# Kernel optimization log

Hardware: AMD Instinct MI355X
Metric: run time of the kernel (lower is better)

Reference implementation:

```python
import jax, jax.numpy as jnp
import numpy as np

D_MODEL = 1024
NUM_TILES = 8
BATCH = 4096
TEMPERATURE = 0.5

gelu = lambda x: jax.nn.gelu(x, approximate=False)  # torch nn.GELU default = exact erf


def setup_inputs() -> dict:
    key = jax.random.key(0)
    ks = jax.random.split(key, 12)
    d, t = D_MODEL, NUM_TILES
    s = lambda fan_in: 1.0 / np.sqrt(fan_in)
    return {
        "x": jax.random.normal(ks[0], (BATCH, d), jnp.float32),
        # router: Linear(d,d) -> GELU -> Linear(d,num_tiles); weights stored (in,out)
        "Wr1": jax.random.uniform(ks[1], (d, d), jnp.float32, -s(d), s(d)),
        "br1": jax.random.uniform(ks[2], (d,), jnp.float32, -s(d), s(d)),
        "Wr2": jax.random.uniform(ks[3], (d, t), jnp.float32, -s(d), s(d)),
        "br2": jax.random.uniform(ks[4], (t,), jnp.float32, -s(d), s(d)),
        # tile nets: Linear(d,2d) -> GELU -> Linear(2d,d), stacked over tiles
        "W1": jax.random.uniform(ks[5], (t, d, 2 * d), jnp.float32, -s(d), s(d)),
        "b1": jax.random.uniform(ks[6], (t, 2 * d), jnp.float32, -s(d), s(d)),
        "W2": jax.random.uniform(ks[7], (t, 2 * d, d), jnp.float32, -s(2 * d), s(2 * d)),
        "b2": jax.random.uniform(ks[8], (t, d), jnp.float32, -s(2 * d), s(2 * d)),
        # output projection Linear(d,d)
        "Wo": jax.random.uniform(ks[9], (d, d), jnp.float32, -s(d), s(d)),
        "bo": jax.random.uniform(ks[10], (d,), jnp.float32, -s(d), s(d)),
    }


def reference(x, Wr1, br1, Wr2, br2, W1, b1, W2, b2, Wo, bo):
    # router logits / temperature
    route_logits = (gelu(x @ Wr1 + br1) @ Wr2 + br2) / TEMPERATURE  # (B, T)
    tile_idx = jnp.argmax(route_logits, axis=-1)                    # (B,)

    # hard routing: compute all tile MLPs, then select the argmax tile per token
    # (dense equivalent of per-sample dispatch; same math as the torch loop)
    h = gelu(jnp.einsum("bd,tdf->btf", x, W1) + b1[None])           # (B, T, 2d)
    tile_out = jnp.einsum("btf,tfd->btd", h, W2) + b2[None]         # (B, T, d)
    selected = jnp.take_along_axis(tile_out, tile_idx[:, None, None], axis=1)[:, 0]  # (B, d)

    output = selected @ Wo + bo                                     # (B, d)
    return output, tile_idx, route_logits
```

## Files before the change

### kernel.cpp

```cpp
#include <hip/hip_runtime.h>
#include <hip/hip_bf16.h>
#include <math.h>
#include <stdint.h>

typedef __bf16 bf16_t;
typedef __bf16 bf16x4 __attribute__((ext_vector_type(4)));
typedef __bf16 bf16x8 __attribute__((ext_vector_type(8)));
typedef float  f32x4  __attribute__((ext_vector_type(4)));

#define BATCH   4096
#define DM      1024
#define DFF     2048
#define NTILES  8
#define MAXXB   40

__device__ __forceinline__ float gelu_exact(float x) {
    return 0.5f * x * (1.0f + erff(x * 0.70710678118654752440f));
}

__device__ __forceinline__ void async_ld16(const bf16_t* g, bf16_t* l) {
    __builtin_amdgcn_global_load_lds(
        (const __attribute__((address_space(1))) void*)g,
        (__attribute__((address_space(3))) void*)l, 16, 0, 0);
}

__device__ __forceinline__ f32x4 mfma16(bf16x8 a, bf16x8 b, f32x4 c) {
    return __builtin_amdgcn_mfma_f32_16x16x32_bf16(a, b, c, 0, 0, 0);
}

template<bool LO>
__device__ void tconv64_body(const float* __restrict__ src, bf16_t* __restrict__ outh,
                             bf16_t* __restrict__ outl, int K, int N, int kt, int nt,
                             float4* t ) {
    const int tid = threadIdx.x;
    const int k0 = kt * 64, n0 = nt * 64;
#pragma unroll
    for (int p = 0; p < 4; ++p) {
        int row = p * 16 + (tid >> 4);
        int c = tid & 15;
        float4 v = *(const float4*)(src + (size_t)(k0 + row) * N + n0 + c * 4);
        t[row * 16 + (c ^ ((row >> 2) & 15))] = v;
    }
    __syncthreads();
    const int n = tid >> 2, b = tid & 3;
    const float* tf = (const float*)t;
    float v[16];
#pragma unroll
    for (int i = 0; i < 16; ++i) {
        int k = 16 * b + i;
        int f4 = k * 16 + ((n >> 2) ^ ((k >> 2) & 15));
        v[i] = tf[f4 * 4 + (n & 3)];
    }
    bf16x8 h0, h1;
#pragma unroll
    for (int i = 0; i < 8; ++i) { h0[i] = (bf16_t)v[i]; h1[i] = (bf16_t)v[8 + i]; }
    size_t oi = (size_t)(n0 + n) * K + k0 + 16 * b;
    *(bf16x8*)(outh + oi) = h0;
    *(bf16x8*)(outh + oi + 8) = h1;
    if constexpr (LO) {
        bf16x8 l0, l1;
#pragma unroll
        for (int i = 0; i < 8; ++i) {
            l0[i] = (bf16_t)(v[i] - (float)h0[i]);
            l1[i] = (bf16_t)(v[8 + i] - (float)h1[i]);
        }
        *(bf16x8*)(outl + oi) = l0;
        *(bf16x8*)(outl + oi + 8) = l1;
    }
}

#define NCVT2 2048
#define NSQ64 256
#define NW1   4096
#define NW2   4096
#define PREP_GRID (NCVT2 + NSQ64 + NSQ64 + NW1 + NW2)

__global__ __launch_bounds__(256) void prep_kernel(
    const float* __restrict__ x, const float* __restrict__ Wr1, const float* __restrict__ Wo,
    const float* __restrict__ W1, const float* __restrict__ W2,
    bf16_t* __restrict__ xh, bf16_t* __restrict__ xl,
    bf16_t* __restrict__ Wr1h, bf16_t* __restrict__ Wr1l, bf16_t* __restrict__ Wot,
    bf16_t* __restrict__ W1t, bf16_t* __restrict__ W2t) {
    __shared__ float4 t[64 * 16];
    int b = blockIdx.x;
    if (b < NCVT2) {
        size_t i = (size_t)b * 256 + threadIdx.x;
        const float4* x4 = (const float4*)x;
        float4 v0 = x4[2 * i], v1 = x4[2 * i + 1];
        float f[8] = {v0.x, v0.y, v0.z, v0.w, v1.x, v1.y, v1.z, v1.w};
        bf16x8 h, l;
#pragma unroll
        for (int j = 0; j < 8; ++j) { h[j] = (bf16_t)f[j]; l[j] = (bf16_t)(f[j] - (float)h[j]); }
        *(bf16x8*)(xh + i * 8) = h;
        *(bf16x8*)(xl + i * 8) = l;
        return;
    }
    b -= NCVT2;
    if (b < NSQ64) { tconv64_body<true >(Wr1, Wr1h, Wr1l, DM, DM, b >> 4, b & 15, t); return; }
    b -= NSQ64;
    if (b < NSQ64) { tconv64_body<false>(Wo, Wot, nullptr, DM, DM, b >> 4, b & 15, t); return; }
    b -= NSQ64;
    if (b < NW1) {
        int mat = b >> 9, r = b & 511;
        size_t off = (size_t)mat * DM * DFF;
        tconv64_body<false>(W1 + off, W1t + off, nullptr, DM, DFF, r >> 5, r & 31, t);
        return;
    }
    b -= NW1;
    {
        int mat = b >> 9, r = b & 511;
        size_t off = (size_t)mat * DM * DFF;
        tconv64_body<false>(W2 + off, W2t + off, nullptr, DFF, DM, r >> 4, r & 15, t);
    }
}

template<bool SPLIT, bool GATHER, bool GELU, bool SCATTER, bool OUTF32>
__global__ __launch_bounds__(512) void gemm_kernel(
    const bf16_t* __restrict__ A, const bf16_t* __restrict__ Alo,
    const bf16_t* __restrict__ Bt, const bf16_t* __restrict__ Btlo,
    const float* __restrict__ bias,
    float* __restrict__ outF, bf16_t* __restrict__ outB,
    const int* __restrict__ perm, const int* __restrict__ counts,
    int M, int N, int K) {
    int tile = 0, rb, cnt = M;
    const int* permT = nullptr;
    if constexpr (GATHER) {
        int xb = blockIdx.x, t = 0, c = 0;
        while (t < NTILES) {
            c = counts[t];
            int nbk = (c + 127) >> 7;
            if (xb < nbk) break;
            xb -= nbk; ++t;
        }
        if (t == NTILES) return;
        tile = t;
        rb = xb * 128;
        cnt = c;
        permT = perm + tile * BATCH;
    } else {
        rb = blockIdx.x * 128;
    }
    Bt   += (size_t)tile * K * N;
    if constexpr (SPLIT) Btlo += (size_t)tile * K * N;
    bias += (size_t)tile * N;

    constexpr int CH  = 128 * 32;
    constexpr int BUF = 2 * CH;
    __shared__ __align__(16) bf16_t As[2 * BUF];
    __shared__ __align__(16) bf16_t Bs[2 * BUF];
    __shared__ __align__(16) bf16_t Asl[SPLIT ? 2 * BUF : 8];
    __shared__ __align__(16) bf16_t Bsl[SPLIT ? 2 * BUF : 8];

    const int lane = threadIdx.x & 63;
    const int wave = threadIdx.x >> 6;
    const int wm = wave & 1, wn = wave >> 1;
    const int nb = blockIdx.y * 128;

    const int srow = lane >> 2;
    const int scol = ((lane & 3) ^ (srow & 3)) * 8;
    const int row = wave * 16 + srow;
    int arow;
    if constexpr (GATHER) {
        int pos = rb + row;
        if (pos > cnt - 1) pos = cnt - 1;
        arow = permT[pos];
    } else {
        arow = rb + row;
    }
    const size_t aoff = (size_t)arow * K + scol;
    const size_t boff = (size_t)(nb + row) * K + scol;

    f32x4 acc[4][2];
#pragma unroll
    for (int i = 0; i < 4; ++i)
#pragma unroll
        for (int j = 0; j < 2; ++j) acc[i][j] = (f32x4){0.f, 0.f, 0.f, 0.f};

    const int lr = lane & 15, lq = lane >> 4;
    const int rdoff = (lr * 4 + (lq ^ (lr & 3))) * 8;

    auto stage = [&](int k0, int buf) {
#pragma unroll
        for (int c = 0; c < 2; ++c) {
            async_ld16(A  + aoff + k0 + c * 32, &As[buf * BUF + c * CH + wave * 512]);
            async_ld16(Bt + boff + k0 + c * 32, &Bs[buf * BUF + c * CH + wave * 512]);
            if constexpr (SPLIT) {
                async_ld16(Alo  + aoff + k0 + c * 32, &Asl[buf * BUF + c * CH + wave * 512]);
                async_ld16(Btlo + boff + k0 + c * 32, &Bsl[buf * BUF + c * CH + wave * 512]);
            }
        }
    };

    auto compute = [&](int cur) {
#pragma unroll
        for (int kk = 0; kk < 2; ++kk) {
            const int base = cur * BUF + kk * CH;
            bf16x8 af[4], bfr[2], afl[4], bfl[2];
#pragma unroll
            for (int i = 0; i < 4; ++i) {
                af[i] = *(const bf16x8*)&As[base + (wm * 4 + i) * 512 + rdoff];
                if constexpr (SPLIT)
                    afl[i] = *(const bf16x8*)&Asl[base + (wm * 4 + i) * 512 + rdoff];
            }
#pragma unroll
            for (int j = 0; j < 2; ++j) {
                bfr[j] = *(const bf16x8*)&Bs[base + (wn * 2 + j) * 512 + rdoff];
                if constexpr (SPLIT)
                    bfl[j] = *(const bf16x8*)&Bsl[base + (wn * 2 + j) * 512 + rdoff];
            }
#pragma unroll
            for (int i = 0; i < 4; ++i)
#pragma unroll
                for (int j = 0; j < 2; ++j) {
                    acc[i][j] = mfma16(af[i], bfr[j], acc[i][j]);
                    if constexpr (SPLIT) {
                        acc[i][j] = mfma16(af[i], bfl[j], acc[i][j]);
                        acc[i][j] = mfma16(afl[i], bfr[j], acc[i][j]);
                    }
                }
        }
    };

    stage(0, 0);
    int cur = 0;
    for (int k0 = 0; k0 < K; k0 += 64, cur ^= 1) {
        __syncthreads();
        if (k0 + 64 < K) stage(k0 + 64, cur ^ 1);
        compute(cur);
    }

#pragma unroll
    for (int i = 0; i < 4; ++i) {
#pragma unroll
        for (int j = 0; j < 2; ++j) {
#pragma unroll
            for (int r = 0; r < 4; ++r) {
                int m = wm * 64 + i * 16 + lq * 4 + r;
                int n = wn * 32 + j * 16 + lr;
                int pos = rb + m;
                if constexpr (GATHER) { if (pos >= cnt) continue; }
                int grow;
                if constexpr (SCATTER) grow = permT[pos];
                else                   grow = pos;
                int gn = nb + n;
                float v = acc[i][j][r] + bias[gn];
                if constexpr (GELU) v = gelu_exact(v);
                if constexpr (OUTF32) outF[(size_t)grow * N + gn] = v;
                else                  outB[(size_t)grow * N + gn] = (bf16_t)v;
            }
        }
    }
}

__global__ __launch_bounds__(256) void router2_kernel(
    const float* __restrict__ Hr, const float* __restrict__ Wr2, const float* __restrict__ br2,
    float* __restrict__ outLog, float* __restrict__ outIdx,
    int* __restrict__ counts, int* __restrict__ perm) {
    __shared__ float w2s[DM * 9];
    __shared__ int h[NTILES], base[NTILES];
    const int tid = threadIdx.x;
    if (tid < NTILES) h[tid] = 0;
    for (int e = tid; e < DM * 8; e += 256) {
        int k = e >> 3, j = e & 7;
        w2s[k * 9 + j] = Wr2[e];
    }
    __syncthreads();

    const int lane = tid & 63, wave = tid >> 6;
    const int sub = lane >> 4;
    const int lr16 = lane & 15;
    const int row = blockIdx.x * 16 + wave * 4 + sub;

    const float4* Hr4 = (const float4*)Hr;
    float acc[8];
#pragma unroll
    for (int j = 0; j < 8; ++j) acc[j] = 0.f;

#pragma unroll
    for (int i = 0; i < 16; ++i) {
        int f = lr16 + i * 16;
        float4 hv = Hr4[(size_t)row * 256 + f];
        float hx[4] = {hv.x, hv.y, hv.z, hv.w};
        int kbase = f * 4;
#pragma unroll
        for (int d = 0; d < 4; ++d) {
            float xv = hx[d];
            const float* w = &w2s[(kbase + d) * 9];
#pragma unroll
            for (int j = 0; j < 8; ++j) acc[j] += xv * w[j];
        }
    }
#pragma unroll
    for (int off = 8; off; off >>= 1)
#pragma unroll
        for (int j = 0; j < 8; ++j) acc[j] += __shfl_down(acc[j], off);

    int bi = 0, rank = 0;
    if (lr16 == 0) {
        float best = -1e30f;
        float lg[8];
#pragma unroll
        for (int j = 0; j < 8; ++j) {
            float v = (acc[j] + br2[j]) * 2.0f;
            lg[j] = v;
            if (v > best) { best = v; bi = j; }
        }
        float4 lo = {lg[0], lg[1], lg[2], lg[3]};
        float4 hi = {lg[4], lg[5], lg[6], lg[7]};
        *(float4*)(outLog + (size_t)row * 8)     = lo;
        *(float4*)(outLog + (size_t)row * 8 + 4) = hi;
        outIdx[row] = (float)bi;
        rank = atomicAdd(&h[bi], 1);
    }
    __syncthreads();
    if (tid < NTILES && h[tid] > 0) base[tid] = atomicAdd(&counts[tid], h[tid]);
    __syncthreads();
    if (lr16 == 0) perm[bi * BATCH + base[bi] + rank] = row;
}

extern "C" void kernel_launch(void* const* d_in, const int* in_sizes, int n_in,
                              void* d_out, int out_size, void* d_ws, size_t ws_size,
                              hipStream_t stream) {
    const float* x   = (const float*)d_in[0];
    const float* Wr1 = (const float*)d_in[1];
    const float* br1 = (const float*)d_in[2];
    const float* Wr2 = (const float*)d_in[3];
    const float* br2 = (const float*)d_in[4];
    const float* W1  = (const float*)d_in[5];
    const float* b1  = (const float*)d_in[6];
    const float* W2  = (const float*)d_in[7];
    const float* b2  = (const float*)d_in[8];
    const float* Wo  = (const float*)d_in[9];
    const float* bo  = (const float*)d_in[10];

    char* ws = (char*)d_ws;
    size_t o = 0;
    auto carve = [&](size_t bytes) { char* p = ws + o; o = (o + bytes + 255) & ~(size_t)255; return p; };
    bf16_t* Wr1h = (bf16_t*)carve((size_t)DM * DM * 2);
    bf16_t* Wr1l = (bf16_t*)carve((size_t)DM * DM * 2);
    bf16_t* Wot  = (bf16_t*)carve((size_t)DM * DM * 2);
    bf16_t* W1t  = (bf16_t*)carve((size_t)NTILES * DM * DFF * 2);
    bf16_t* W2t  = (bf16_t*)carve((size_t)NTILES * DM * DFF * 2);
    bf16_t* xh   = (bf16_t*)carve((size_t)BATCH * DM * 2);
    bf16_t* xl   = (bf16_t*)carve((size_t)BATCH * DM * 2);
    bf16_t* H1   = (bf16_t*)carve((size_t)BATCH * DFF * 2);
    bf16_t* sel  = (bf16_t*)carve((size_t)BATCH * DM * 2);
    float*  Hr   = (float*)carve((size_t)BATCH * DM * 4);
    int*    counts = (int*)carve(NTILES * sizeof(int));
    int*    perm   = (int*)carve((size_t)NTILES * BATCH * sizeof(int));

    float* outMain = (float*)d_out;
    float* outIdx  = outMain + (size_t)BATCH * DM;
    float* outLog  = outIdx + BATCH;

    hipMemsetAsync(counts, 0, NTILES * sizeof(int), stream);

    prep_kernel<<<PREP_GRID, 256, 0, stream>>>(x, Wr1, Wo, W1, W2,
                                               xh, xl, Wr1h, Wr1l, Wot, W1t, W2t);

    gemm_kernel<true, false, true, false, true><<<dim3(BATCH / 128, DM / 128, 1), 512, 0, stream>>>(
        xh, xl, Wr1h, Wr1l, br1, Hr, nullptr, nullptr, nullptr, BATCH, DM, DM);

    router2_kernel<<<BATCH / 16, 256, 0, stream>>>(Hr, Wr2, br2, outLog, outIdx, counts, perm);

    gemm_kernel<false, true, true, true, false><<<dim3(MAXXB, DFF / 128, 1), 512, 0, stream>>>(
        xh, nullptr, W1t, nullptr, b1, nullptr, H1, perm, counts, BATCH, DFF, DM);

    gemm_kernel<false, true, false, true, false><<<dim3(MAXXB, DM / 128, 1), 512, 0, stream>>>(
        H1, nullptr, W2t, nullptr, b2, nullptr, sel, perm, counts, BATCH, DM, DFF);

    gemm_kernel<false, false, false, false, true><<<dim3(BATCH / 128, DM / 128, 1), 512, 0, stream>>>(
        sel, nullptr, Wot, nullptr, bo, outMain, nullptr, nullptr, nullptr, BATCH, DM, DM);
}
```

Baseline: 367.4 us.

## Overlap router GEMM with tile-weight transpose conversion in one fused launch

```diff
diff --git a/kernel.cpp b/kernel.cpp
--- a/kernel.cpp
+++ b/kernel.cpp
@@ -4,7 +4,6 @@
 #include <stdint.h>
 
 typedef __bf16 bf16_t;
-typedef __bf16 bf16x4 __attribute__((ext_vector_type(4)));
 typedef __bf16 bf16x8 __attribute__((ext_vector_type(8)));
 typedef float  f32x4  __attribute__((ext_vector_type(4)));
 
@@ -31,8 +30,7 @@
 template<bool LO>
 __device__ void tconv64_body(const float* __restrict__ src, bf16_t* __restrict__ outh,
                              bf16_t* __restrict__ outl, int K, int N, int kt, int nt,
-                             float4* t ) {
-    const int tid = threadIdx.x;
+                             float4* t , int tid) {
     const int k0 = kt * 64, n0 = nt * 64;
 #pragma unroll
     for (int p = 0; p < 4; ++p) {
@@ -70,17 +68,12 @@
 }
 
 #define NCVT2 2048
-#define NSQ64 256
-#define NW1   4096
-#define NW2   4096
-#define PREP_GRID (NCVT2 + NSQ64 + NSQ64 + NW1 + NW2)
-
-__global__ __launch_bounds__(256) void prep_kernel(
-    const float* __restrict__ x, const float* __restrict__ Wr1, const float* __restrict__ Wo,
-    const float* __restrict__ W1, const float* __restrict__ W2,
+#define PREP_A_GRID (NCVT2 + 256)
+
+__global__ __launch_bounds__(256) void prep_a_kernel(
+    const float* __restrict__ x, const float* __restrict__ Wr1,
     bf16_t* __restrict__ xh, bf16_t* __restrict__ xl,
-    bf16_t* __restrict__ Wr1h, bf16_t* __restrict__ Wr1l, bf16_t* __restrict__ Wot,
-    bf16_t* __restrict__ W1t, bf16_t* __restrict__ W2t) {
+    bf16_t* __restrict__ Wr1h, bf16_t* __restrict__ Wr1l) {
     __shared__ float4 t[64 * 16];
     int b = blockIdx.x;
     if (b < NCVT2) {
@@ -96,36 +89,26 @@
         return;
     }
     b -= NCVT2;
-    if (b < NSQ64) { tconv64_body<true >(Wr1, Wr1h, Wr1l, DM, DM, b >> 4, b & 15, t); return; }
-    b -= NSQ64;
-    if (b < NSQ64) { tconv64_body<false>(Wo, Wot, nullptr, DM, DM, b >> 4, b & 15, t); return; }
-    b -= NSQ64;
-    if (b < NW1) {
-        int mat = b >> 9, r = b & 511;
-        size_t off = (size_t)mat * DM * DFF;
-        tconv64_body<false>(W1 + off, W1t + off, nullptr, DM, DFF, r >> 5, r & 31, t);
-        return;
-    }
-    b -= NW1;
-    {
-        int mat = b >> 9, r = b & 511;
-        size_t off = (size_t)mat * DM * DFF;
-        tconv64_body<false>(W2 + off, W2t + off, nullptr, DFF, DM, r >> 4, r & 15, t);
-    }
-}
-
-template<bool SPLIT, bool GATHER, bool GELU, bool SCATTER, bool OUTF32>
-__global__ __launch_bounds__(512) void gemm_kernel(
+    tconv64_body<true>(Wr1, Wr1h, Wr1l, DM, DM, b >> 4, b & 15, t, threadIdx.x);
+}
+
+template<bool SPLIT, bool GATHER, bool GELU, bool SCATTER, bool OUTF32, int BK>
+__device__ __forceinline__ void gemm_body(
     const bf16_t* __restrict__ A, const bf16_t* __restrict__ Alo,
     const bf16_t* __restrict__ Bt, const bf16_t* __restrict__ Btlo,
     const float* __restrict__ bias,
     float* __restrict__ outF, bf16_t* __restrict__ outB,
     const int* __restrict__ perm, const int* __restrict__ counts,
-    int M, int N, int K) {
+    int M, int N, int K, int bx, int by,
+    bf16_t* As, bf16_t* Bs, bf16_t* Asl, bf16_t* Bsl) {
+    constexpr int NCH = BK / 32;
+    constexpr int CH  = 128 * 32;
+    constexpr int BUF = NCH * CH;
+
     int tile = 0, rb, cnt = M;
     const int* permT = nullptr;
     if constexpr (GATHER) {
-        int xb = blockIdx.x, t = 0, c = 0;
+        int xb = bx, t = 0, c = 0;
         while (t < NTILES) {
             c = counts[t];
             int nbk = (c + 127) >> 7;
@@ -138,23 +121,16 @@
         cnt = c;
         permT = perm + tile * BATCH;
     } else {
-        rb = blockIdx.x * 128;
+        rb = bx * 128;
     }
     Bt   += (size_t)tile * K * N;
     if constexpr (SPLIT) Btlo += (size_t)tile * K * N;
     bias += (size_t)tile * N;
 
-    constexpr int CH  = 128 * 32;
-    constexpr int BUF = 2 * CH;
-    __shared__ __align__(16) bf16_t As[2 * BUF];
-    __shared__ __align__(16) bf16_t Bs[2 * BUF];
-    __shared__ __align__(16) bf16_t Asl[SPLIT ? 2 * BUF : 8];
-    __shared__ __align__(16) bf16_t Bsl[SPLIT ? 2 * BUF : 8];
-
     const int lane = threadIdx.x & 63;
     const int wave = threadIdx.x >> 6;
     const int wm = wave & 1, wn = wave >> 1;
-    const int nb = blockIdx.y * 128;
+    const int nb = by * 128;
 
     const int srow = lane >> 2;
     const int scol = ((lane & 3) ^ (srow & 3)) * 8;
@@ -181,7 +157,7 @@
 
     auto stage = [&](int k0, int buf) {
 #pragma unroll
-        for (int c = 0; c < 2; ++c) {
+        for (int c = 0; c < NCH; ++c) {
             async_ld16(A  + aoff + k0 + c * 32, &As[buf * BUF + c * CH + wave * 512]);
             async_ld16(Bt + boff + k0 + c * 32, &Bs[buf * BUF + c * CH + wave * 512]);
             if constexpr (SPLIT) {
@@ -193,7 +169,7 @@
 
     auto compute = [&](int cur) {
 #pragma unroll
-        for (int kk = 0; kk < 2; ++kk) {
+        for (int kk = 0; kk < NCH; ++kk) {
             const int base = cur * BUF + kk * CH;
             bf16x8 af[4], bfr[2], afl[4], bfl[2];
 #pragma unroll
@@ -223,9 +199,9 @@
 
     stage(0, 0);
     int cur = 0;
-    for (int k0 = 0; k0 < K; k0 += 64, cur ^= 1) {
+    for (int k0 = 0; k0 < K; k0 += BK, cur ^= 1) {
         __syncthreads();
-        if (k0 + 64 < K) stage(k0 + 64, cur ^ 1);
+        if (k0 + BK < K) stage(k0 + BK, cur ^ 1);
         compute(cur);
     }
 
@@ -250,6 +226,63 @@
             }
         }
     }
+}
+
+#define NTCONV_TILES (4096 + 4096 + 256)
+#define R1F_GRID (256 + NTCONV_TILES / 2)
+
+__global__ __launch_bounds__(512) void r1_fused_kernel(
+    const bf16_t* __restrict__ xh, const bf16_t* __restrict__ xl,
+    const bf16_t* __restrict__ Wr1h, const bf16_t* __restrict__ Wr1l,
+    const float* __restrict__ br1, float* __restrict__ Hr,
+    const float* __restrict__ W1, const float* __restrict__ W2,
+    const float* __restrict__ Wo,
+    bf16_t* __restrict__ W1t, bf16_t* __restrict__ W2t, bf16_t* __restrict__ Wot) {
+    __shared__ __align__(16) bf16_t smem[32768];
+    const int bid = blockIdx.x;
+    if (bid < 256) {
+        gemm_body<true, false, true, false, true, 32>(
+            xh, xl, Wr1h, Wr1l, br1, Hr, nullptr, nullptr, nullptr,
+            BATCH, DM, DM, bid & 31, bid >> 5,
+            smem, smem + 8192, smem + 16384, smem + 24576);
+        return;
+    }
+    const int tix = bid - 256;
+    const int half = threadIdx.x >> 8;
+    const int tid = threadIdx.x & 255;
+    float4* t = (float4*)smem + half * 1024;
+    const int tile = tix * 2 + half;
+    if (tile < 4096) {
+        int mat = tile >> 9, r = tile & 511;
+        size_t off = (size_t)mat * DM * DFF;
+        tconv64_body<false>(W1 + off, W1t + off, nullptr, DM, DFF, r >> 5, r & 31, t, tid);
+    } else if (tile < 8192) {
+        int tt = tile - 4096;
+        int mat = tt >> 9, r = tt & 511;
+        size_t off = (size_t)mat * DM * DFF;
+        tconv64_body<false>(W2 + off, W2t + off, nullptr, DFF, DM, r >> 4, r & 15, t, tid);
+    } else {
+        int r = tile - 8192;
+        tconv64_body<false>(Wo, Wot, nullptr, DM, DM, r >> 4, r & 15, t, tid);
+    }
+}
+
+template<bool SPLIT, bool GATHER, bool GELU, bool SCATTER, bool OUTF32>
+__global__ __launch_bounds__(512) void gemm_kernel(
+    const bf16_t* __restrict__ A, const bf16_t* __restrict__ Alo,
+    const bf16_t* __restrict__ Bt, const bf16_t* __restrict__ Btlo,
+    const float* __restrict__ bias,
+    float* __restrict__ outF, bf16_t* __restrict__ outB,
+    const int* __restrict__ perm, const int* __restrict__ counts,
+    int M, int N, int K) {
+    constexpr int E = 2 * 2 * 128 * 32;
+    __shared__ __align__(16) bf16_t As[E];
+    __shared__ __align__(16) bf16_t Bs[E];
+    __shared__ __align__(16) bf16_t Asl[SPLIT ? E : 8];
+    __shared__ __align__(16) bf16_t Bsl[SPLIT ? E : 8];
+    gemm_body<SPLIT, GATHER, GELU, SCATTER, OUTF32, 64>(
+        A, Alo, Bt, Btlo, bias, outF, outB, perm, counts,
+        M, N, K, blockIdx.x, blockIdx.y, As, Bs, Asl, Bsl);
 }
 
 __global__ __launch_bounds__(256) void router2_kernel(
@@ -355,11 +388,10 @@
 
     hipMemsetAsync(counts, 0, NTILES * sizeof(int), stream);
 
-    prep_kernel<<<PREP_GRID, 256, 0, stream>>>(x, Wr1, Wo, W1, W2,
-                                               xh, xl, Wr1h, Wr1l, Wot, W1t, W2t);
-
-    gemm_kernel<true, false, true, false, true><<<dim3(BATCH / 128, DM / 128, 1), 512, 0, stream>>>(
-        xh, xl, Wr1h, Wr1l, br1, Hr, nullptr, nullptr, nullptr, BATCH, DM, DM);
+    prep_a_kernel<<<PREP_A_GRID, 256, 0, stream>>>(x, Wr1, xh, xl, Wr1h, Wr1l);
+
+    r1_fused_kernel<<<R1F_GRID, 512, 0, stream>>>(xh, xl, Wr1h, Wr1l, br1, Hr,
+                                                  W1, W2, Wo, W1t, W2t, Wot);
 
     router2_kernel<<<BATCH / 16, 256, 0, stream>>>(Hr, Wr2, br2, outLog, outIdx, counts, perm);
 
```

After: 340.1 us. 1.08x faster.
